# Kernel tuning notes

Hardware: AMD Instinct MI355X
Metric: run time of the kernel (lower is better)

The kernel has to match this reference:

```python
import jax, jax.numpy as jnp
import numpy as np

N = 50000       # nodes
E = 800000      # edges
IN = 64         # input node feature dim
H = 4           # attention heads
C = 32          # per-head channels (h_dim)
HC = H * C      # 128, concat output per conv
ED = 16         # edge feature dim
G = 2000        # number of graphs (molecules)
NEG = 0.2       # GATConv negative slope


def setup_inputs() -> dict:
    key = jax.random.key(0)
    ks = jax.random.split(key, 40)
    rn = lambda k, shp, s=0.1: (jax.random.normal(k, shp, jnp.float32) * s)
    inp = {}
    inp["x"] = jax.random.normal(ks[0], (N, IN), jnp.float32)
    inp["edge_index"] = jax.random.randint(ks[1], (2, E), 0, N)
    inp["edge_attr"] = jax.random.normal(ks[2], (E, ED), jnp.float32)
    inp["batch"] = jnp.sort(jax.random.randint(ks[3], (N,), 0, G))
    dins = [IN, HC, HC]
    i = 4
    for l in (1, 2, 3):
        din = dins[l - 1]
        inp[f"W{l}"] = rn(ks[i], (din, HC)); i += 1
        inp[f"as{l}"] = rn(ks[i], (H, C)); i += 1
        inp[f"ad{l}"] = rn(ks[i], (H, C)); i += 1
        inp[f"We{l}"] = rn(ks[i], (ED, HC)); i += 1
        inp[f"ae{l}"] = rn(ks[i], (H, C)); i += 1
        inp[f"b{l}"] = rn(ks[i], (HC,)); i += 1
    D = 4 * HC
    inp["lw1"] = rn(ks[i], (D, D)); i += 1
    inp["lb1"] = rn(ks[i], (D,)); i += 1
    inp["lw2"] = rn(ks[i], (D, 1)); i += 1
    inp["lb2"] = rn(ks[i], (1,)); i += 1
    return inp


def gat_conv(x, src, dst, edge_attr, W, a_s, a_d, We, a_e, b):
    n = x.shape[0]
    h = (x @ W).reshape(n, H, C)                       # [N,H,C]
    alpha_src = (h * a_s).sum(-1)                      # [N,H]
    alpha_dst = (h * a_d).sum(-1)                      # [N,H]
    he = (edge_attr @ We).reshape(-1, H, C)            # [E,H,C]
    alpha_edge = (he * a_e).sum(-1)                    # [E,H]
    alpha = jax.nn.leaky_relu(alpha_src[src] + alpha_dst[dst] + alpha_edge, NEG)
    # per-destination softmax over incoming edges (stable)
    amax = jax.ops.segment_max(alpha, dst, num_segments=n)
    amax = jnp.where(jnp.isfinite(amax), amax, 0.0)
    ex = jnp.exp(alpha - amax[dst])                    # [E,H]
    denom = jax.ops.segment_sum(ex, dst, num_segments=n)
    w = ex / (denom[dst] + 1e-16)                      # [E,H]
    m = h[src] * w[:, :, None]                         # [E,H,C]
    out = jax.ops.segment_sum(m, dst, num_segments=n)  # [N,H,C]
    return out.reshape(n, HC) + b


def reference(x, edge_index, edge_attr, batch,
              W1, as1, ad1, We1, ae1, b1,
              W2, as2, ad2, We2, ae2, b2,
              W3, as3, ad3, We3, ae3, b3,
              lw1, lb1, lw2, lb2):
    src, dst = edge_index[0], edge_index[1]
    h1 = gat_conv(x, src, dst, edge_attr, W1, as1, ad1, We1, ae1, b1)
    h2 = gat_conv(h1, src, dst, edge_attr, W2, as2, ad2, We2, ae2, b2)
    h3 = gat_conv(h2, src, dst, edge_attr, W3, as3, ad3, We3, ae3, b3)
    h_pool = jax.ops.segment_sum(h3, batch, num_segments=G)  # global_add_pool
    h_pool_ = h_pool[batch]                                  # == repeat_interleave by counts
    h = jnp.concatenate([h1, h2, h3, h_pool_], axis=1)       # [N, 4*HC]
    h = jax.nn.leaky_relu(h @ lw1 + lb1, 0.01)               # torch LeakyReLU default
    return h @ lw2 + lb2                                     # [N, 1]
```

## Files before the change

### kernel.cpp

```cpp
#include <hip/hip_runtime.h>
#include <hip/hip_bf16.h>
#include <math.h>

#define NN 50000
#define NE 800000
#define DIN1 64
#define NHEAD 4
#define CH 32
#define HC 128
#define EDIM 16
#define NG 2000
#define SP 56
#define MAXCH 64

typedef __attribute__((ext_vector_type(8))) short short8;
typedef __attribute__((ext_vector_type(4))) float floatx4;

__device__ __forceinline__ float lrelu(float x, float s) { return x > 0.f ? x : s * x; }

__device__ __forceinline__ unsigned short f2bf(float x) {
  unsigned int u = __float_as_uint(x);
  u += 0x7fff + ((u >> 16) & 1);
  return (unsigned short)(u >> 16);
}
__device__ __forceinline__ float bflo(unsigned int u) { return __uint_as_float(u << 16); }
__device__ __forceinline__ float bfhi(unsigned int u) { return __uint_as_float(u & 0xffff0000u); }

__global__ __launch_bounds__(256) void k_we_a(
    const float* __restrict__ We1, const float* __restrict__ ae1,
    const float* __restrict__ We2, const float* __restrict__ ae2,
    const float* __restrict__ We3, const float* __restrict__ ae3,
    float* __restrict__ we_a) {
  int t = threadIdx.x;
  if (t >= 3 * EDIM * NHEAD) return;
  int l = t / (EDIM * NHEAD);
  int rem = t % (EDIM * NHEAD);
  int d = rem / NHEAD, h = rem % NHEAD;
  const float* We = (l == 0) ? We1 : ((l == 1) ? We2 : We3);
  const float* ae = (l == 0) ? ae1 : ((l == 1) ? ae2 : ae3);
  float s = 0.f;
  for (int c = 0; c < CH; ++c) s += We[d * HC + h * CH + c] * ae[h * CH + c];
  we_a[t] = s;
}

__global__ __launch_bounds__(256) void k_lw1t(const float* __restrict__ lw1, unsigned short* __restrict__ lw1tb) {
  int i = blockIdx.x * 256 + threadIdx.x;
  if (i >= 512 * 384) return;
  int n = i / 384, k = i % 384;
  lw1tb[i] = f2bf(lw1[(size_t)k * 512 + n]);
}

__global__ __launch_bounds__(256) void k_wt(const float* __restrict__ W1, const float* __restrict__ W2,
                                            const float* __restrict__ W3, unsigned short* __restrict__ wtb) {
  int i = blockIdx.x * 256 + threadIdx.x;
  if (i < 128 * 64) {
    int j = i / 64, k = i % 64;
    wtb[i] = f2bf(W1[k * HC + j]);
  } else if (i < 128 * 64 + 128 * 128) {
    int ii = i - 128 * 64;
    int j = ii / 128, k = ii % 128;
    wtb[i] = f2bf(W2[k * HC + j]);
  } else if (i < 128 * 64 + 2 * 128 * 128) {
    int ii = i - (128 * 64 + 128 * 128);
    int j = ii / 128, k = ii % 128;
    wtb[i] = f2bf(W3[k * HC + j]);
  }
}

__global__ __launch_bounds__(256) void k_cast(const float* __restrict__ x, unsigned short* __restrict__ xb0) {
  int i = blockIdx.x * 256 + threadIdx.x;
  if (i < NN * DIN1) xb0[i] = f2bf(x[i]);
}

__global__ __launch_bounds__(256) void k_hist(const int* __restrict__ dst, int* __restrict__ cnt) {
  int e = blockIdx.x * 256 + threadIdx.x;
  if (e < NE) atomicAdd(&cnt[dst[e]], 1);
}

__global__ __launch_bounds__(256) void k_scan1(const int* __restrict__ cnt, int* __restrict__ row_start,
                                               int* __restrict__ aux) {
  __shared__ int s[256];
  int t = threadIdx.x;
  int i = blockIdx.x * 256 + t;
  int v = (i < NN) ? cnt[i] : 0;
  s[t] = v;
  __syncthreads();
  for (int off = 1; off < 256; off <<= 1) {
    int tv = (t >= off) ? s[t - off] : 0;
    __syncthreads();
    s[t] += tv;
    __syncthreads();
  }
  if (i < NN) row_start[i] = s[t] - v;
  if (t == 255) aux[blockIdx.x] = s[255];
}

__global__ __launch_bounds__(256) void k_scan2(int* __restrict__ aux, int nb) {
  __shared__ int s[256];
  int t = threadIdx.x;
  int v = (t < nb) ? aux[t] : 0;
  s[t] = v;
  __syncthreads();
  for (int off = 1; off < 256; off <<= 1) {
    int tv = (t >= off) ? s[t - off] : 0;
    __syncthreads();
    s[t] += tv;
    __syncthreads();
  }
  if (t < nb) aux[t] = s[t] - v;
}

__global__ __launch_bounds__(256) void k_scan3(int* __restrict__ row_start, const int* __restrict__ aux) {
  int i = blockIdx.x * 256 + threadIdx.x;
  if (i < NN) row_start[i] += aux[i >> 8];
  else if (i == NN) row_start[NN] = NE;
}

__global__ __launch_bounds__(256) void k_scatter(const int* __restrict__ dst, const int* __restrict__ row_start,
                                                 int* __restrict__ fill, int* __restrict__ perm) {
  int e = blockIdx.x * 256 + threadIdx.x;
  if (e >= NE) return;
  int d = dst[e];
  int p = atomicAdd(&fill[d], 1);
  perm[row_start[d] + p] = e;
}

__global__ __launch_bounds__(256) void k_permute(const int* __restrict__ perm, const int* __restrict__ src,
                                                 const float* __restrict__ edge_attr, const float* __restrict__ wea,
                                                 int* __restrict__ srcp, float* __restrict__ aep) {
  __shared__ float wl[3 * EDIM * NHEAD];
  int t = threadIdx.x;
  if (t < 3 * EDIM * NHEAD) wl[t] = wea[t];
  __syncthreads();
  int pos = blockIdx.x * 256 + t;
  if (pos >= NE) return;
  int e = perm[pos];
  srcp[pos] = src[e];
  float ea[EDIM];
#pragma unroll
  for (int k = 0; k < EDIM; k += 4) {
    float4 v = *(const float4*)&edge_attr[(size_t)e * EDIM + k];
    ea[k] = v.x; ea[k + 1] = v.y; ea[k + 2] = v.z; ea[k + 3] = v.w;
  }
#pragma unroll
  for (int l = 0; l < 3; ++l) {
    float a0 = 0.f, a1 = 0.f, a2 = 0.f, a3 = 0.f;
#pragma unroll
    for (int k = 0; k < EDIM; ++k) {
      float ev = ea[k];
      a0 += ev * wl[l * 64 + k * 4 + 0];
      a1 += ev * wl[l * 64 + k * 4 + 1];
      a2 += ev * wl[l * 64 + k * 4 + 2];
      a3 += ev * wl[l * 64 + k * 4 + 3];
    }
    *(float4*)&aep[(size_t)l * NE * 4 + (size_t)pos * 4] = make_float4(a0, a1, a2, a3);
  }
}

__global__ __launch_bounds__(256) void k_gstart(const int* __restrict__ batch, int* __restrict__ gs) {
  int i = blockIdx.x * 256 + threadIdx.x;
  if (i >= NN) return;
  int b = batch[i];
  if (i == 0) {
    for (int g = 0; g <= b; ++g) gs[g] = 0;
  } else {
    int pb = batch[i - 1];
    for (int g = pb + 1; g <= b; ++g) gs[g] = i;
  }
  if (i == NN - 1) {
    for (int g = b + 1; g <= NG; ++g) gs[g] = NN;
  }
}

template <int K, int ASTRIDE>
__global__ __launch_bounds__(256) void k_conv_mfma(const unsigned short* __restrict__ xin,
                                                   const unsigned short* __restrict__ wt,
                                                   const float* __restrict__ a_s, const float* __restrict__ a_d,
                                                   unsigned short* __restrict__ htb,
                                                   float* __restrict__ asrc, float* __restrict__ adst) {
  __shared__ unsigned short As[128 * SP];
  __shared__ unsigned short Bs[128 * SP];
  __shared__ float ss[HC], sd[HC];
  int t = threadIdx.x;
  int n0 = blockIdx.x * 128;
  int lane = t & 63;
  int wave = t >> 6;
  int wr = wave >> 1, wc = wave & 1;
  if (t < HC) ss[t] = a_s[t];
  else if (t < 2 * HC) sd[t - HC] = a_d[t - HC];

  floatx4 acc[4][4];
#pragma unroll
  for (int a = 0; a < 4; ++a)
#pragma unroll
    for (int b = 0; b < 4; ++b) acc[a][b] = (floatx4){0.f, 0.f, 0.f, 0.f};

  int sm = t & 127;
  int sc = (t >> 7) * 16;
  bool arow_ok = (n0 + sm) < NN;
  const unsigned short* aglob = xin + (size_t)(n0 + sm) * ASTRIDE + sc;
  const unsigned short* bglob = wt + sm * K + sc;
  unsigned short* asl = As + sm * SP + sc;
  unsigned short* bsl = Bs + sm * SP + sc;

  int frow = lane & 15, fk = (lane >> 4) * 8;
  const unsigned short* arow = As + (wr * 64 + frow) * SP + fk;
  const unsigned short* brow = Bs + (wc * 64 + frow) * SP + fk;

  for (int k0 = 0; k0 < K; k0 += 32) {
    uint4 a0 = arow_ok ? *(const uint4*)(aglob) : make_uint4(0, 0, 0, 0);
    uint4 a1 = arow_ok ? *(const uint4*)(aglob + 8) : make_uint4(0, 0, 0, 0);
    uint4 b0 = *(const uint4*)(bglob);
    uint4 b1 = *(const uint4*)(bglob + 8);
    aglob += 32;
    bglob += 32;
    __syncthreads();
    *(uint4*)(asl) = a0;
    *(uint4*)(asl + 8) = a1;
    *(uint4*)(bsl) = b0;
    *(uint4*)(bsl + 8) = b1;
    __syncthreads();
    short8 af[4], bf[4];
#pragma unroll
    for (int ti = 0; ti < 4; ++ti) af[ti] = *(const short8*)(arow + ti * 16 * SP);
#pragma unroll
    for (int tj = 0; tj < 4; ++tj) bf[tj] = *(const short8*)(brow + tj * 16 * SP);
#pragma unroll
    for (int ti = 0; ti < 4; ++ti)
#pragma unroll
      for (int tj = 0; tj < 4; ++tj)
        acc[ti][tj] = __builtin_amdgcn_mfma_f32_16x16x32_bf16(af[ti], bf[tj], acc[ti][tj], 0, 0, 0);
  }

  int q = lane & 15;
  int colg = wc * 64 + q;
  int hb = wc * 2;
#pragma unroll
  for (int ti = 0; ti < 4; ++ti) {
    int rowb = n0 + wr * 64 + ti * 16 + (lane >> 4) * 4;
#pragma unroll
    for (int r = 0; r < 4; ++r) {
      int row = rowb + r;
      float v0 = acc[ti][0][r], v1 = acc[ti][1][r], v2 = acc[ti][2][r], v3 = acc[ti][3][r];
      if (row < NN) {
        htb[(size_t)row * HC + colg] = f2bf(v0);
        htb[(size_t)row * HC + colg + 16] = f2bf(v1);
        htb[(size_t)row * HC + colg + 32] = f2bf(v2);
        htb[(size_t)row * HC + colg + 48] = f2bf(v3);
      }
      float s0 = v0 * ss[colg] + v1 * ss[colg + 16];
      float s1 = v2 * ss[colg + 32] + v3 * ss[colg + 48];
      float dd0 = v0 * sd[colg] + v1 * sd[colg + 16];
      float dd1 = v2 * sd[colg + 32] + v3 * sd[colg + 48];
#pragma unroll
      for (int m = 1; m < 16; m <<= 1) {
        s0 += __shfl_xor(s0, m, 16);
        s1 += __shfl_xor(s1, m, 16);
        dd0 += __shfl_xor(dd0, m, 16);
        dd1 += __shfl_xor(dd1, m, 16);
      }
      if (q == 0 && row < NN) {
        asrc[row * 4 + hb] = s0;
        asrc[row * 4 + hb + 1] = s1;
        adst[row * 4 + hb] = dd0;
        adst[row * 4 + hb + 1] = dd1;
      }
    }
  }
}

__global__ __launch_bounds__(256) void k_aggregate(
    const unsigned short* __restrict__ htb, const int* __restrict__ srcp,
    const float* __restrict__ aep, const float* __restrict__ asrc, const float* __restrict__ adst,
    const int* __restrict__ row_start, const float* __restrict__ bias,
    unsigned short* __restrict__ xb, int col0) {
  __shared__ float exs[4][MAXCH][4];
  __shared__ int cns[4];
  int t = threadIdx.x;
  int lane = t & 63, wid = t >> 6;
  int n = blockIdx.x * 4 + wid;
  bool nok = n < NN;
  int rs = nok ? row_start[n] : 0;
  int re = nok ? row_start[n + 1] : 0;
  int deg = re - rs;
  if (lane == 0) cns[wid] = (deg + MAXCH - 1) / MAXCH;
  __syncthreads();
  int maxc = max(max(cns[0], cns[1]), max(cns[2], cns[3]));
  int q = lane & 15, g = lane >> 4;
  int h = q >> 2;
  float4 ad4 = nok ? *(const float4*)&adst[n * 4] : make_float4(0.f, 0.f, 0.f, 0.f);
  float acc[8];
#pragma unroll
  for (int j = 0; j < 8; ++j) acc[j] = 0.f;
  float d0 = 0.f, d1 = 0.f, d2 = 0.f, d3 = 0.f;

  for (int cc = 0; cc < maxc; ++cc) {
    int base = rs + cc * MAXCH;
    int m = re - base;
    if (m > MAXCH) m = MAXCH;
    if (lane < m) {
      int i = base + lane;
      int s = srcp[i];
      float4 ae = *(const float4*)&aep[(size_t)i * 4];
      float4 as4 = *(const float4*)&asrc[s * 4];
      float4 ex;
      ex.x = __expf(lrelu(as4.x + ad4.x + ae.x, 0.2f));
      ex.y = __expf(lrelu(as4.y + ad4.y + ae.y, 0.2f));
      ex.z = __expf(lrelu(as4.z + ad4.z + ae.z, 0.2f));
      ex.w = __expf(lrelu(as4.w + ad4.w + ae.w, 0.2f));
      *(float4*)&exs[wid][lane][0] = ex;
      d0 += ex.x; d1 += ex.y; d2 += ex.z; d3 += ex.w;
    }
    __syncthreads();
    int iters = (m > 0) ? ((m + 3) >> 2) : 0;
    for (int kk = 0; kk < iters; ++kk) {
      int ii = kk * 4 + g;
      if (ii < m) {
        int i = base + ii;
        int s = srcp[i];
        float w = exs[wid][ii][h];
        uint4 hv = *(const uint4*)(htb + (size_t)s * HC + q * 8);
        acc[0] += w * bflo(hv.x);
        acc[1] += w * bfhi(hv.x);
        acc[2] += w * bflo(hv.y);
        acc[3] += w * bfhi(hv.y);
        acc[4] += w * bflo(hv.z);
        acc[5] += w * bfhi(hv.z);
        acc[6] += w * bflo(hv.w);
        acc[7] += w * bfhi(hv.w);
      }
    }
    __syncthreads();
  }

#pragma unroll
  for (int mm = 1; mm < 64; mm <<= 1) {
    d0 += __shfl_xor(d0, mm, 64);
    d1 += __shfl_xor(d1, mm, 64);
    d2 += __shfl_xor(d2, mm, 64);
    d3 += __shfl_xor(d3, mm, 64);
  }
#pragma unroll
  for (int j = 0; j < 8; ++j) {
    acc[j] += __shfl_xor(acc[j], 16, 64);
    acc[j] += __shfl_xor(acc[j], 32, 64);
  }
  if (nok && g == 0) {
    float dh = (h == 0) ? d0 : ((h == 1) ? d1 : ((h == 2) ? d2 : d3));
    float inv = 1.f / (dh + 1e-16f);
    unsigned int w[4];
#pragma unroll
    for (int j = 0; j < 4; ++j) {
      float v0 = acc[2 * j] * inv + bias[q * 8 + 2 * j];
      float v1 = acc[2 * j + 1] * inv + bias[q * 8 + 2 * j + 1];
      w[j] = (unsigned int)f2bf(v0) | ((unsigned int)f2bf(v1) << 16);
    }
    *(uint4*)&xb[(size_t)n * 384 + col0 + q * 8] = make_uint4(w[0], w[1], w[2], w[3]);
  }
}

__global__ __launch_bounds__(128) void k_pool(const unsigned short* __restrict__ xb, const int* __restrict__ gs,
                                              float* __restrict__ hpool) {
  int g = blockIdx.x;
  int j = threadIdx.x;
  int s = gs[g], e = gs[g + 1];
  float acc = 0.f;
  for (int i = s; i < e; ++i) acc += bflo((unsigned int)xb[(size_t)i * 384 + 256 + j]);
  hpool[(size_t)g * HC + j] = acc;
}

__global__ __launch_bounds__(256) void k_pool_gemm(const float* __restrict__ hpool, const float* __restrict__ lw1,
                                                   float* __restrict__ ph) {
  __shared__ float hp[16][128];
  int t = threadIdx.x;
  int j0 = blockIdx.x * 128;
  int g0 = blockIdx.y * 16;
  int jj = t & 127, gg = t >> 7;
#pragma unroll
  for (int i = 0; i < 8; ++i) {
    int q = t + 256 * i;
    int row = q >> 7, col = q & 127;
    hp[row][col] = hpool[(size_t)(g0 + row) * HC + col];
  }
  __syncthreads();
  float acc[8];
#pragma unroll
  for (int i = 0; i < 8; ++i) acc[i] = 0.f;
  for (int k = 0; k < HC; ++k) {
    float wv = lw1[(size_t)(384 + k) * 512 + j0 + jj];
#pragma unroll
    for (int gi = 0; gi < 8; ++gi) acc[gi] += hp[gg + 2 * gi][k] * wv;
  }
#pragma unroll
  for (int gi = 0; gi < 8; ++gi) ph[(size_t)(g0 + gg + 2 * gi) * 512 + j0 + jj] = acc[gi];
}

__global__ __launch_bounds__(256) void k_outinit(float* __restrict__ out, const float* __restrict__ lb2) {
  int i = blockIdx.x * 256 + threadIdx.x;
  if (i < NN) out[i] = lb2[0];
}

__global__ __launch_bounds__(256) void k_mlp_mfma(
    const unsigned short* __restrict__ xb, const unsigned short* __restrict__ lw1tb,
    const float* __restrict__ ph, const int* __restrict__ batch,
    const float* __restrict__ lb1, const float* __restrict__ lw2,
    float* __restrict__ out) {
  __shared__ unsigned short As[128 * SP];
  __shared__ unsigned short Bs[128 * SP];
  int t = threadIdx.x;
  int j0 = blockIdx.x * 128;
  int n0 = blockIdx.y * 128;
  int lane = t & 63;
  int wave = t >> 6;
  int wr = wave >> 1, wc = wave & 1;

  floatx4 acc[4][4];
#pragma unroll
  for (int a = 0; a < 4; ++a)
#pragma unroll
    for (int b = 0; b < 4; ++b) acc[a][b] = (floatx4){0.f, 0.f, 0.f, 0.f};

  int sm = t & 127;
  int sc = (t >> 7) * 16;
  bool arow_ok = (n0 + sm) < NN;
  const unsigned short* aglob = xb + (size_t)(n0 + sm) * 384 + sc;
  const unsigned short* bglob = lw1tb + (size_t)(j0 + sm) * 384 + sc;
  unsigned short* asl = As + sm * SP + sc;
  unsigned short* bsl = Bs + sm * SP + sc;

  int frow = lane & 15, fk = (lane >> 4) * 8;
  const unsigned short* arow = As + (wr * 64 + frow) * SP + fk;
  const unsigned short* brow = Bs + (wc * 64 + frow) * SP + fk;

  for (int k0 = 0; k0 < 384; k0 += 32) {
    uint4 a0 = arow_ok ? *(const uint4*)(aglob) : make_uint4(0, 0, 0, 0);
    uint4 a1 = arow_ok ? *(const uint4*)(aglob + 8) : make_uint4(0, 0, 0, 0);
    uint4 b0 = *(const uint4*)(bglob);
    uint4 b1 = *(const uint4*)(bglob + 8);
    aglob += 32;
    bglob += 32;
    __syncthreads();
    *(uint4*)(asl) = a0;
    *(uint4*)(asl + 8) = a1;
    *(uint4*)(bsl) = b0;
    *(uint4*)(bsl + 8) = b1;
    __syncthreads();
    short8 af[4], bf[4];
#pragma unroll
    for (int ti = 0; ti < 4; ++ti) af[ti] = *(const short8*)(arow + ti * 16 * SP);
#pragma unroll
    for (int tj = 0; tj < 4; ++tj) bf[tj] = *(const short8*)(brow + tj * 16 * SP);
#pragma unroll
    for (int ti = 0; ti < 4; ++ti)
#pragma unroll
      for (int tj = 0; tj < 4; ++tj)
        acc[ti][tj] = __builtin_amdgcn_mfma_f32_16x16x32_bf16(af[ti], bf[tj], acc[ti][tj], 0, 0, 0);
  }

  int colg = j0 + wc * 64 + (lane & 15);
#pragma unroll
  for (int ti = 0; ti < 4; ++ti) {
    int rowb = n0 + wr * 64 + ti * 16 + (lane >> 4) * 4;
#pragma unroll
    for (int r = 0; r < 4; ++r) {
      int row = rowb + r;
      int rc = (row < NN) ? row : 0;
      int bg = batch[rc];
      float partial = 0.f;
#pragma unroll
      for (int tj = 0; tj < 4; ++tj) {
        int j = colg + tj * 16;
        float v = acc[ti][tj][r] + ph[(size_t)bg * 512 + j] + lb1[j];
        partial += lrelu(v, 0.01f) * lw2[j];
      }
#pragma unroll
      for (int m = 1; m < 16; m <<= 1) partial += __shfl_xor(partial, m, 16);
      if ((lane & 15) == 0 && row < NN) atomicAdd(&out[row], partial);
    }
  }
}

extern "C" void kernel_launch(void* const* d_in, const int* in_sizes, int n_in,
                              void* d_out, int out_size, void* d_ws, size_t ws_size,
                              hipStream_t stream) {
  const float* x = (const float*)d_in[0];
  const int* edge_index = (const int*)d_in[1];
  const int* src = edge_index;
  const int* dstp = edge_index + NE;
  const float* edge_attr = (const float*)d_in[2];
  const int* batch = (const int*)d_in[3];
  const float* W[3] = {(const float*)d_in[4], (const float*)d_in[10], (const float*)d_in[16]};
  const float* as_[3] = {(const float*)d_in[5], (const float*)d_in[11], (const float*)d_in[17]};
  const float* ad_[3] = {(const float*)d_in[6], (const float*)d_in[12], (const float*)d_in[18]};
  const float* We_[3] = {(const float*)d_in[7], (const float*)d_in[13], (const float*)d_in[19]};
  const float* ae_[3] = {(const float*)d_in[8], (const float*)d_in[14], (const float*)d_in[20]};
  const float* b_[3] = {(const float*)d_in[9], (const float*)d_in[15], (const float*)d_in[21]};
  const float* lw1 = (const float*)d_in[22];
  const float* lb1 = (const float*)d_in[23];
  const float* lw2 = (const float*)d_in[24];
  const float* lb2 = (const float*)d_in[25];
  float* out = (float*)d_out;

  float* f = (float*)d_ws;
  size_t o = 0;
  float* asrc = f + o;  o += (size_t)NN * NHEAD;
  float* adst = f + o;  o += (size_t)NN * NHEAD;
  float* wea = f + o;   o += 256;
  float* hpool = f + o; o += (size_t)NG * HC;
  float* ph = f + o;    o += (size_t)NG * 512;
  float* aep = f + o;   o += (size_t)3 * NE * 4;
  unsigned short* xb0 = (unsigned short*)(f + o);   o += (size_t)NN * DIN1 / 2;
  unsigned short* htb = (unsigned short*)(f + o);   o += (size_t)NN * HC / 2;
  unsigned short* xb = (unsigned short*)(f + o);    o += (size_t)NN * 384 / 2;
  unsigned short* wtb = (unsigned short*)(f + o);   o += (size_t)(128 * 64 + 2 * 128 * 128) / 2;
  unsigned short* lw1tb = (unsigned short*)(f + o); o += (512 * 384) / 2;
  int* row_start = (int*)(f + o);
  int* cnt = row_start + (NN + 1);
  int* fill = cnt + NN;
  int* aux = fill + NN;
  int* gs = aux + 256;
  int* perm = gs + (NG + 1);
  int* srcp = perm + NE;

  const int NB = (NN + 255) / 256;
  const int EB = (NE + 255) / 256;

  hipMemsetAsync(cnt, 0, (size_t)2 * NN * sizeof(int), stream);

  k_we_a<<<1, 256, 0, stream>>>(We_[0], ae_[0], We_[1], ae_[1], We_[2], ae_[2], wea);
  k_lw1t<<<(512 * 384 + 255) / 256, 256, 0, stream>>>(lw1, lw1tb);
  k_wt<<<(128 * 64 + 2 * 128 * 128 + 255) / 256, 256, 0, stream>>>(W[0], W[1], W[2], wtb);
  k_cast<<<(NN * DIN1 + 255) / 256, 256, 0, stream>>>(x, xb0);
  k_hist<<<EB, 256, 0, stream>>>(dstp, cnt);
  k_scan1<<<NB, 256, 0, stream>>>(cnt, row_start, aux);
  k_scan2<<<1, 256, 0, stream>>>(aux, NB);
  k_scan3<<<NB, 256, 0, stream>>>(row_start, aux);
  k_scatter<<<EB, 256, 0, stream>>>(dstp, row_start, fill, perm);
  k_permute<<<EB, 256, 0, stream>>>(perm, src, edge_attr, wea, srcp, aep);
  k_gstart<<<NB, 256, 0, stream>>>(batch, gs);
  k_outinit<<<NB, 256, 0, stream>>>(out, lb2);

  const int CONVB = (NN + 127) / 128;
  unsigned short* wt_l[3] = {wtb, wtb + 128 * 64, wtb + 128 * 64 + 128 * 128};
  for (int l = 0; l < 3; ++l) {
    if (l == 0)
      k_conv_mfma<64, 64><<<CONVB, 256, 0, stream>>>(xb0, wt_l[0], as_[0], ad_[0], htb, asrc, adst);
    else if (l == 1)
      k_conv_mfma<128, 384><<<CONVB, 256, 0, stream>>>(xb, wt_l[1], as_[1], ad_[1], htb, asrc, adst);
    else
      k_conv_mfma<128, 384><<<CONVB, 256, 0, stream>>>(xb + 128, wt_l[2], as_[2], ad_[2], htb, asrc, adst);
    k_aggregate<<<(NN + 3) / 4, 256, 0, stream>>>(htb, srcp, aep + (size_t)l * NE * 4, asrc, adst,
                                                  row_start, b_[l], xb, l * HC);
  }

  k_pool<<<NG, 128, 0, stream>>>(xb, gs, hpool);
  k_pool_gemm<<<dim3(4, NG / 16), 256, 0, stream>>>(hpool, lw1, ph);
  k_mlp_mfma<<<dim3(4, (NN + 127) / 128), 256, 0, stream>>>(xb, lw1tb, ph, batch, lb1, lw2, out);
}
```

Before: 597.7 us.

## Fold attention logits into conv MFMA, unroll aggregate gather, async-LDS MLP GEMM

Precomputes W·a_s and W·a_d as an extra bf16 weight block so the conv kernel gets alpha_src and alpha_dst from extra MFMAs instead of a shuffle reduction. The aggregate loop now processes two edges per iteration with clamped indices to raise memory-level parallelism. The MLP GEMM is rewritten with 256-wide output tiles, global_load_lds async copies into LDS and a launch-bounds occupancy hint, halving grid columns. The logits now go through bf16 rounding of the folded weights, which changes precision slightly, and the new MLP path uses more registers per thread.

```diff
diff --git a/kernel.cpp b/kernel.cpp
--- a/kernel.cpp
+++ b/kernel.cpp
@@ -12,6 +12,7 @@
 #define NG 2000
 #define SP 56
 #define MAXCH 64
+#define MJ 256
 
 typedef __attribute__((ext_vector_type(8))) short short8;
 typedef __attribute__((ext_vector_type(4))) float floatx4;
@@ -25,6 +26,11 @@
 }
 __device__ __forceinline__ float bflo(unsigned int u) { return __uint_as_float(u << 16); }
 __device__ __forceinline__ float bfhi(unsigned int u) { return __uint_as_float(u & 0xffff0000u); }
+
+__device__ __forceinline__ void async16(void* lds, const void* g) {
+  __builtin_amdgcn_global_load_lds((const __attribute__((address_space(1))) unsigned int*)g,
+                                   (__attribute__((address_space(3))) unsigned int*)lds, 16, 0, 0);
+}
 
 __global__ __launch_bounds__(256) void k_we_a(
     const float* __restrict__ We1, const float* __restrict__ ae1,
@@ -41,6 +47,26 @@
   float s = 0.f;
   for (int c = 0; c < CH; ++c) s += We[d * HC + h * CH + c] * ae[h * CH + c];
   we_a[t] = s;
+}
+
+__global__ __launch_bounds__(256) void k_wsd(
+    const float* __restrict__ W1, const float* __restrict__ as1, const float* __restrict__ ad1,
+    const float* __restrict__ W2, const float* __restrict__ as2, const float* __restrict__ ad2,
+    const float* __restrict__ W3, const float* __restrict__ as3, const float* __restrict__ ad3,
+    unsigned short* __restrict__ wsdb) {
+  int i = blockIdx.x * 256 + threadIdx.x;
+  if (i >= 3 * 16 * 128) return;
+  int l = i >> 11;
+  int col = (i >> 7) & 15;
+  int k = i & 127;
+  if (col >= 8 || (l == 0 && k >= DIN1)) { wsdb[i] = 0; return; }
+  const float* W = (l == 0) ? W1 : ((l == 1) ? W2 : W3);
+  int head = col & 3;
+  const float* av = (col < 4) ? ((l == 0) ? as1 : ((l == 1) ? as2 : as3))
+                              : ((l == 0) ? ad1 : ((l == 1) ? ad2 : ad3));
+  float s = 0.f;
+  for (int c = 0; c < CH; ++c) s += W[(size_t)k * HC + head * CH + c] * av[head * CH + c];
+  wsdb[i] = f2bf(s);
 }
 
 __global__ __launch_bounds__(256) void k_lw1t(const float* __restrict__ lw1, unsigned short* __restrict__ lw1tb) {
@@ -175,43 +201,48 @@
 template <int K, int ASTRIDE>
 __global__ __launch_bounds__(256) void k_conv_mfma(const unsigned short* __restrict__ xin,
                                                    const unsigned short* __restrict__ wt,
-                                                   const float* __restrict__ a_s, const float* __restrict__ a_d,
+                                                   const unsigned short* __restrict__ wsd,
                                                    unsigned short* __restrict__ htb,
                                                    float* __restrict__ asrc, float* __restrict__ adst) {
   __shared__ unsigned short As[128 * SP];
   __shared__ unsigned short Bs[128 * SP];
-  __shared__ float ss[HC], sd[HC];
+  __shared__ unsigned short Bs2[16 * SP];
   int t = threadIdx.x;
   int n0 = blockIdx.x * 128;
   int lane = t & 63;
   int wave = t >> 6;
   int wr = wave >> 1, wc = wave & 1;
-  if (t < HC) ss[t] = a_s[t];
-  else if (t < 2 * HC) sd[t - HC] = a_d[t - HC];
 
   floatx4 acc[4][4];
-#pragma unroll
-  for (int a = 0; a < 4; ++a)
+  floatx4 acce[4];
+#pragma unroll
+  for (int a = 0; a < 4; ++a) {
+    acce[a] = (floatx4){0.f, 0.f, 0.f, 0.f};
 #pragma unroll
     for (int b = 0; b < 4; ++b) acc[a][b] = (floatx4){0.f, 0.f, 0.f, 0.f};
+  }
 
   int sm = t & 127;
   int sc = (t >> 7) * 16;
-  bool arow_ok = (n0 + sm) < NN;
-  const unsigned short* aglob = xin + (size_t)(n0 + sm) * ASTRIDE + sc;
+  int arow = n0 + sm;
+  if (arow >= NN) arow = NN - 1;
+  const unsigned short* aglob = xin + (size_t)arow * ASTRIDE + sc;
   const unsigned short* bglob = wt + sm * K + sc;
   unsigned short* asl = As + sm * SP + sc;
   unsigned short* bsl = Bs + sm * SP + sc;
 
   int frow = lane & 15, fk = (lane >> 4) * 8;
-  const unsigned short* arow = As + (wr * 64 + frow) * SP + fk;
-  const unsigned short* brow = Bs + (wc * 64 + frow) * SP + fk;
+  const unsigned short* arow_p = As + (wr * 64 + frow) * SP + fk;
+  const unsigned short* brow_p = Bs + (wc * 64 + frow) * SP + fk;
+  const unsigned short* b2row_p = Bs2 + frow * SP + fk;
 
   for (int k0 = 0; k0 < K; k0 += 32) {
-    uint4 a0 = arow_ok ? *(const uint4*)(aglob) : make_uint4(0, 0, 0, 0);
-    uint4 a1 = arow_ok ? *(const uint4*)(aglob + 8) : make_uint4(0, 0, 0, 0);
+    uint4 a0 = *(const uint4*)(aglob);
+    uint4 a1 = *(const uint4*)(aglob + 8);
     uint4 b0 = *(const uint4*)(bglob);
     uint4 b1 = *(const uint4*)(bglob + 8);
+    uint4 b2 = make_uint4(0, 0, 0, 0);
+    if (t < 64) b2 = *(const uint4*)(wsd + (t >> 2) * 128 + k0 + (t & 3) * 8);
     aglob += 32;
     bglob += 32;
     __syncthreads();
@@ -219,51 +250,45 @@
     *(uint4*)(asl + 8) = a1;
     *(uint4*)(bsl) = b0;
     *(uint4*)(bsl + 8) = b1;
+    if (t < 64) *(uint4*)(Bs2 + (t >> 2) * SP + (t & 3) * 8) = b2;
     __syncthreads();
     short8 af[4], bf[4];
 #pragma unroll
-    for (int ti = 0; ti < 4; ++ti) af[ti] = *(const short8*)(arow + ti * 16 * SP);
-#pragma unroll
-    for (int tj = 0; tj < 4; ++tj) bf[tj] = *(const short8*)(brow + tj * 16 * SP);
+    for (int ti = 0; ti < 4; ++ti) af[ti] = *(const short8*)(arow_p + ti * 16 * SP);
+#pragma unroll
+    for (int tj = 0; tj < 4; ++tj) bf[tj] = *(const short8*)(brow_p + tj * 16 * SP);
 #pragma unroll
     for (int ti = 0; ti < 4; ++ti)
 #pragma unroll
       for (int tj = 0; tj < 4; ++tj)
         acc[ti][tj] = __builtin_amdgcn_mfma_f32_16x16x32_bf16(af[ti], bf[tj], acc[ti][tj], 0, 0, 0);
+    if (wc == 0) {
+      short8 bf2 = *(const short8*)(b2row_p);
+#pragma unroll
+      for (int ti = 0; ti < 4; ++ti)
+        acce[ti] = __builtin_amdgcn_mfma_f32_16x16x32_bf16(af[ti], bf2, acce[ti], 0, 0, 0);
+    }
+    arow_p += 0;
   }
 
   int q = lane & 15;
   int colg = wc * 64 + q;
-  int hb = wc * 2;
 #pragma unroll
   for (int ti = 0; ti < 4; ++ti) {
     int rowb = n0 + wr * 64 + ti * 16 + (lane >> 4) * 4;
 #pragma unroll
     for (int r = 0; r < 4; ++r) {
       int row = rowb + r;
-      float v0 = acc[ti][0][r], v1 = acc[ti][1][r], v2 = acc[ti][2][r], v3 = acc[ti][3][r];
       if (row < NN) {
-        htb[(size_t)row * HC + colg] = f2bf(v0);
-        htb[(size_t)row * HC + colg + 16] = f2bf(v1);
-        htb[(size_t)row * HC + colg + 32] = f2bf(v2);
-        htb[(size_t)row * HC + colg + 48] = f2bf(v3);
-      }
-      float s0 = v0 * ss[colg] + v1 * ss[colg + 16];
-      float s1 = v2 * ss[colg + 32] + v3 * ss[colg + 48];
-      float dd0 = v0 * sd[colg] + v1 * sd[colg + 16];
-      float dd1 = v2 * sd[colg + 32] + v3 * sd[colg + 48];
-#pragma unroll
-      for (int m = 1; m < 16; m <<= 1) {
-        s0 += __shfl_xor(s0, m, 16);
-        s1 += __shfl_xor(s1, m, 16);
-        dd0 += __shfl_xor(dd0, m, 16);
-        dd1 += __shfl_xor(dd1, m, 16);
-      }
-      if (q == 0 && row < NN) {
-        asrc[row * 4 + hb] = s0;
-        asrc[row * 4 + hb + 1] = s1;
-        adst[row * 4 + hb] = dd0;
-        adst[row * 4 + hb + 1] = dd1;
+        htb[(size_t)row * HC + colg] = f2bf(acc[ti][0][r]);
+        htb[(size_t)row * HC + colg + 16] = f2bf(acc[ti][1][r]);
+        htb[(size_t)row * HC + colg + 32] = f2bf(acc[ti][2][r]);
+        htb[(size_t)row * HC + colg + 48] = f2bf(acc[ti][3][r]);
+        if (wc == 0 && q < 8) {
+          float v = acce[ti][r];
+          if (q < 4) asrc[row * 4 + q] = v;
+          else adst[row * 4 + (q - 4)] = v;
+        }
       }
     }
   }
@@ -312,23 +337,26 @@
       d0 += ex.x; d1 += ex.y; d2 += ex.z; d3 += ex.w;
     }
     __syncthreads();
-    int iters = (m > 0) ? ((m + 3) >> 2) : 0;
+    int iters = (m > 0) ? ((m + 7) >> 3) : 0;
     for (int kk = 0; kk < iters; ++kk) {
-      int ii = kk * 4 + g;
-      if (ii < m) {
-        int i = base + ii;
-        int s = srcp[i];
-        float w = exs[wid][ii][h];
-        uint4 hv = *(const uint4*)(htb + (size_t)s * HC + q * 8);
-        acc[0] += w * bflo(hv.x);
-        acc[1] += w * bfhi(hv.x);
-        acc[2] += w * bflo(hv.y);
-        acc[3] += w * bfhi(hv.y);
-        acc[4] += w * bflo(hv.z);
-        acc[5] += w * bfhi(hv.z);
-        acc[6] += w * bflo(hv.w);
-        acc[7] += w * bfhi(hv.w);
-      }
+      int ii0 = kk * 8 + g;
+      int ii1 = ii0 + 4;
+      int i0 = base + ((ii0 < m) ? ii0 : 0);
+      int i1 = base + ((ii1 < m) ? ii1 : 0);
+      int s0 = srcp[i0];
+      int s1 = srcp[i1];
+      uint4 h0 = *(const uint4*)(htb + (size_t)s0 * HC + q * 8);
+      uint4 h1 = *(const uint4*)(htb + (size_t)s1 * HC + q * 8);
+      float w0 = (ii0 < m) ? exs[wid][ii0][h] : 0.f;
+      float w1 = (ii1 < m) ? exs[wid][ii1][h] : 0.f;
+      acc[0] += w0 * bflo(h0.x) + w1 * bflo(h1.x);
+      acc[1] += w0 * bfhi(h0.x) + w1 * bfhi(h1.x);
+      acc[2] += w0 * bflo(h0.y) + w1 * bflo(h1.y);
+      acc[3] += w0 * bfhi(h0.y) + w1 * bfhi(h1.y);
+      acc[4] += w0 * bflo(h0.z) + w1 * bflo(h1.z);
+      acc[5] += w0 * bfhi(h0.z) + w1 * bfhi(h1.z);
+      acc[6] += w0 * bflo(h0.w) + w1 * bflo(h1.w);
+      acc[7] += w0 * bfhi(h0.w) + w1 * bfhi(h1.w);
     }
     __syncthreads();
   }
@@ -400,64 +428,67 @@
   if (i < NN) out[i] = lb2[0];
 }
 
-__global__ __launch_bounds__(256) void k_mlp_mfma(
+__global__ __launch_bounds__(256, 2) void k_mlp_mfma(
     const unsigned short* __restrict__ xb, const unsigned short* __restrict__ lw1tb,
     const float* __restrict__ ph, const int* __restrict__ batch,
     const float* __restrict__ lb1, const float* __restrict__ lw2,
     float* __restrict__ out) {
-  __shared__ unsigned short As[128 * SP];
-  __shared__ unsigned short Bs[128 * SP];
-  int t = threadIdx.x;
-  int j0 = blockIdx.x * 128;
+  __shared__ unsigned short As[4 * 128 * 8];
+  __shared__ unsigned short Bs[4 * 256 * 8];
+  int t = threadIdx.x;
+  int j0 = blockIdx.x * MJ;
   int n0 = blockIdx.y * 128;
   int lane = t & 63;
   int wave = t >> 6;
   int wr = wave >> 1, wc = wave & 1;
 
-  floatx4 acc[4][4];
+  floatx4 acc[4][8];
 #pragma unroll
   for (int a = 0; a < 4; ++a)
 #pragma unroll
-    for (int b = 0; b < 4; ++b) acc[a][b] = (floatx4){0.f, 0.f, 0.f, 0.f};
-
-  int sm = t & 127;
-  int sc = (t >> 7) * 16;
-  bool arow_ok = (n0 + sm) < NN;
-  const unsigned short* aglob = xb + (size_t)(n0 + sm) * 384 + sc;
-  const unsigned short* bglob = lw1tb + (size_t)(j0 + sm) * 384 + sc;
-  unsigned short* asl = As + sm * SP + sc;
-  unsigned short* bsl = Bs + sm * SP + sc;
-
-  int frow = lane & 15, fk = (lane >> 4) * 8;
-  const unsigned short* arow = As + (wr * 64 + frow) * SP + fk;
-  const unsigned short* brow = Bs + (wc * 64 + frow) * SP + fk;
-
-  for (int k0 = 0; k0 < 384; k0 += 32) {
-    uint4 a0 = arow_ok ? *(const uint4*)(aglob) : make_uint4(0, 0, 0, 0);
-    uint4 a1 = arow_ok ? *(const uint4*)(aglob + 8) : make_uint4(0, 0, 0, 0);
-    uint4 b0 = *(const uint4*)(bglob);
-    uint4 b1 = *(const uint4*)(bglob + 8);
-    aglob += 32;
-    bglob += 32;
-    __syncthreads();
-    *(uint4*)(asl) = a0;
-    *(uint4*)(asl + 8) = a1;
-    *(uint4*)(bsl) = b0;
-    *(uint4*)(bsl + 8) = b1;
-    __syncthreads();
-    short8 af[4], bf[4];
-#pragma unroll
-    for (int ti = 0; ti < 4; ++ti) af[ti] = *(const short8*)(arow + ti * 16 * SP);
-#pragma unroll
-    for (int tj = 0; tj < 4; ++tj) bf[tj] = *(const short8*)(brow + tj * 16 * SP);
+    for (int b = 0; b < 8; ++b) acc[a][b] = (floatx4){0.f, 0.f, 0.f, 0.f};
+
+  int arow = n0 + (t & 127);
+  if (arow >= NN) arow = NN - 1;
+  const unsigned short* agp = xb + (size_t)arow * 384 + (t >> 7) * 8;
+  const unsigned short* bgp = lw1tb + (size_t)(j0 + t) * 384;
+  unsigned short* asb0 = As + (size_t)(wave * 64) * 8;
+  unsigned short* asb1 = As + (size_t)(wave * 64 + 256) * 8;
+  unsigned short* bsb[4];
+#pragma unroll
+  for (int p = 0; p < 4; ++p) bsb[p] = Bs + (size_t)(p * 256 + wave * 64) * 8;
+
+  async16(asb0, agp);
+  async16(asb1, agp + 16);
+#pragma unroll
+  for (int p = 0; p < 4; ++p) async16(bsb[p], bgp + p * 8);
+
+  const unsigned short* afp = As + ((size_t)(lane >> 4) * 128 + wr * 64 + (lane & 15)) * 8;
+  const unsigned short* bfp = Bs + ((size_t)(lane >> 4) * 256 + wc * 128 + (lane & 15)) * 8;
+
+  for (int kk = 0; kk < 12; ++kk) {
+    __syncthreads();
+    short8 af[4], bf[8];
+#pragma unroll
+    for (int ti = 0; ti < 4; ++ti) af[ti] = *(const short8*)(afp + (size_t)ti * 16 * 8);
+#pragma unroll
+    for (int tj = 0; tj < 8; ++tj) bf[tj] = *(const short8*)(bfp + (size_t)tj * 16 * 8);
+    __syncthreads();
+    if (kk < 11) {
+      int k0 = (kk + 1) * 32;
+      async16(asb0, agp + k0);
+      async16(asb1, agp + k0 + 16);
+#pragma unroll
+      for (int p = 0; p < 4; ++p) async16(bsb[p], bgp + k0 + p * 8);
+    }
 #pragma unroll
     for (int ti = 0; ti < 4; ++ti)
 #pragma unroll
-      for (int tj = 0; tj < 4; ++tj)
+      for (int tj = 0; tj < 8; ++tj)
         acc[ti][tj] = __builtin_amdgcn_mfma_f32_16x16x32_bf16(af[ti], bf[tj], acc[ti][tj], 0, 0, 0);
   }
 
-  int colg = j0 + wc * 64 + (lane & 15);
+  int colg = j0 + wc * 128 + (lane & 15);
 #pragma unroll
   for (int ti = 0; ti < 4; ++ti) {
     int rowb = n0 + wr * 64 + ti * 16 + (lane >> 4) * 4;
@@ -468,7 +499,7 @@
       int bg = batch[rc];
       float partial = 0.f;
 #pragma unroll
-      for (int tj = 0; tj < 4; ++tj) {
+      for (int tj = 0; tj < 8; ++tj) {
         int j = colg + tj * 16;
         float v = acc[ti][tj][r] + ph[(size_t)bg * 512 + j] + lb1[j];
         partial += lrelu(v, 0.01f) * lw2[j];
@@ -514,6 +545,7 @@
   unsigned short* xb = (unsigned short*)(f + o);    o += (size_t)NN * 384 / 2;
   unsigned short* wtb = (unsigned short*)(f + o);   o += (size_t)(128 * 64 + 2 * 128 * 128) / 2;
   unsigned short* lw1tb = (unsigned short*)(f + o); o += (512 * 384) / 2;
+  unsigned short* wsdb = (unsigned short*)(f + o);  o += (size_t)(3 * 16 * 128) / 2;
   int* row_start = (int*)(f + o);
   int* cnt = row_start + (NN + 1);
   int* fill = cnt + NN;
@@ -528,6 +560,8 @@
   hipMemsetAsync(cnt, 0, (size_t)2 * NN * sizeof(int), stream);
 
   k_we_a<<<1, 256, 0, stream>>>(We_[0], ae_[0], We_[1], ae_[1], We_[2], ae_[2], wea);
+  k_wsd<<<(3 * 16 * 128 + 255) / 256, 256, 0, stream>>>(W[0], as_[0], ad_[0], W[1], as_[1], ad_[1],
+                                                        W[2], as_[2], ad_[2], wsdb);
   k_lw1t<<<(512 * 384 + 255) / 256, 256, 0, stream>>>(lw1, lw1tb);
   k_wt<<<(128 * 64 + 2 * 128 * 128 + 255) / 256, 256, 0, stream>>>(W[0], W[1], W[2], wtb);
   k_cast<<<(NN * DIN1 + 255) / 256, 256, 0, stream>>>(x, xb0);
@@ -543,17 +577,18 @@
   const int CONVB = (NN + 127) / 128;
   unsigned short* wt_l[3] = {wtb, wtb + 128 * 64, wtb + 128 * 64 + 128 * 128};
   for (int l = 0; l < 3; ++l) {
+    unsigned short* wsd_l = wsdb + (size_t)l * 16 * 128;
     if (l == 0)
-      k_conv_mfma<64, 64><<<CONVB, 256, 0, stream>>>(xb0, wt_l[0], as_[0], ad_[0], htb, asrc, adst);
+      k_conv_mfma<64, 64><<<CONVB, 256, 0, stream>>>(xb0, wt_l[0], wsd_l, htb, asrc, adst);
     else if (l == 1)
-      k_conv_mfma<128, 384><<<CONVB, 256, 0, stream>>>(xb, wt_l[1], as_[1], ad_[1], htb, asrc, adst);
+      k_conv_mfma<128, 384><<<CONVB, 256, 0, stream>>>(xb, wt_l[1], wsd_l, htb, asrc, adst);
     else
-      k_conv_mfma<128, 384><<<CONVB, 256, 0, stream>>>(xb + 128, wt_l[2], as_[2], ad_[2], htb, asrc, adst);
+      k_conv_mfma<128, 384><<<CONVB, 256, 0, stream>>>(xb + 128, wt_l[2], wsd_l, htb, asrc, adst);
     k_aggregate<<<(NN + 3) / 4, 256, 0, stream>>>(htb, srcp, aep + (size_t)l * NE * 4, asrc, adst,
                                                   row_start, b_[l], xb, l * HC);
   }
 
   k_pool<<<NG, 128, 0, stream>>>(xb, gs, hpool);
   k_pool_gemm<<<dim3(4, NG / 16), 256, 0, stream>>>(hpool, lw1, ph);
-  k_mlp_mfma<<<dim3(4, (NN + 127) / 128), 256, 0, stream>>>(xb, lw1tb, ph, batch, lb1, lw2, out);
-}
+  k_mlp_mfma<<<dim3(2, (NN + 127) / 128), 256, 0, stream>>>(xb, lw1tb, ph, batch, lb1, lw2, out);
+}
```

New measurement: 559.8 us. 6.3% less time.
